# Kernel tuning notes

Measured on AMD Instinct MI355X. Metric: run time of the kernel, lower is better.

The kernel has to match this reference:

```python
import jax, jax.numpy as jnp
import numpy as np

EPS = 1.1920929e-07  # torch.finfo(float32).eps, RMSNorm default eps

def _rms(x, w):
    return x * jax.lax.rsqrt(jnp.mean(x * x, axis=-1, keepdims=True) + EPS) * w

def setup_inputs() -> dict:
    key = jax.random.key(0)
    ks = jax.random.split(key, 8)
    V, E, M, L, B, T = 4096, 1024, 4096, 2, 32, 256
    s = 0.02
    return {
        "tokens": jax.random.randint(ks[0], (B, T), 0, V),
        "targets": jax.random.randint(ks[1], (B, T), 0, V),
        "emb_w": jax.random.normal(ks[2], (V, E), jnp.float32) * s,
        "block_norm_w": jax.random.normal(ks[3], (L, E), jnp.float32) * s,
        "fc1_w": jax.random.normal(ks[4], (L, M, E), jnp.float32) * s,
        "fc1_b": jnp.zeros((L, M), jnp.float32),
        "fc2_w": jax.random.normal(ks[5], (L, E, M), jnp.float32) * s,
        "fc2_b": jnp.zeros((L, E), jnp.float32),
        "norm_w": jax.random.normal(ks[6], (E,), jnp.float32) * s,
        "cur_w": jax.random.normal(ks[7], (E, E), jnp.float32) * s,
        "cur_b": jnp.zeros((E,), jnp.float32),
        "nxt_w": jax.random.normal(jax.random.fold_in(key, 99), (E, E), jnp.float32) * s,
        "nxt_b": jnp.zeros((E,), jnp.float32),
    }

def reference(tokens, targets, emb_w, block_norm_w, fc1_w, fc1_b, fc2_w, fc2_b,
              norm_w, cur_w, cur_b, nxt_w, nxt_b):
    B, T = tokens.shape
    E = emb_w.shape[1]
    L = block_norm_w.shape[0]
    embeds = emb_w[tokens]  # [B,T,E]

    def step(inp, xs):
        tok_emb, tok, tgt = xs  # [B,E], [B], [B]
        inp = tok_emb + inp
        h = inp
        for l in range(L):  # fixed small layer count
            y = jax.nn.silu(_rms(h, block_norm_w[l]) @ fc1_w[l].T + fc1_b[l])
            h = h + y @ fc2_w[l].T + fc2_b[l]
        x = _rms(inp + h, norm_w)
        cur_emb = x @ cur_w.T + cur_b
        nxt_emb = x @ nxt_w.T + nxt_b
        cur_logit = cur_emb @ emb_w.T  # [B,V]
        nxt_logit = nxt_emb @ emb_w.T
        lp_cur = jax.nn.log_softmax(cur_logit, axis=-1)
        lp_nxt = jax.nn.log_softmax(nxt_logit, axis=-1)
        ce_cur = -jnp.mean(jnp.take_along_axis(lp_cur, tok[:, None], axis=1))
        ce_nxt = -jnp.mean(jnp.take_along_axis(lp_nxt, tgt[:, None], axis=1))
        ce = (ce_cur + ce_nxt) / 2
        aux = jnp.mean((cur_emb - inp) ** 2)
        return nxt_emb, (nxt_logit, ce, aux)

    xs = (jnp.swapaxes(embeds, 0, 1), tokens.T, targets.T)
    init = jnp.zeros((B, E), embeds.dtype)
    _, (logits, ces, auxs) = jax.lax.scan(step, init, xs)
    return jnp.swapaxes(logits, 0, 1), jnp.mean(ces), jnp.mean(auxs)
```

## Files before the change

kernel.cpp:

```cpp
#include <hip/hip_runtime.h>
#include <math.h>

#define TT  256
#define BB  32
#define EE  1024
#define MM  4096
#define VV  4096
#define BE  (BB*EE)
#define NROWS (TT*BB)
#define EPSF 1.1920929e-07f

typedef _Float16 h2 __attribute__((ext_vector_type(2)));

__device__ inline float dot2f(h2 a, h2 b, float c) {
#if __has_builtin(__builtin_amdgcn_fdot2)
  return __builtin_amdgcn_fdot2(a, b, c, false);
#else
  return c + (float)a[0] * (float)b[0] + (float)a[1] * (float)b[1];
#endif
}

__device__ inline unsigned ldb_u32(const unsigned* p) {
  return __hip_atomic_load((unsigned*)p, __ATOMIC_RELAXED, __HIP_MEMORY_SCOPE_AGENT);
}
__device__ inline void stb_u32(unsigned* p, unsigned v) {
  __hip_atomic_store(p, v, __ATOMIC_RELAXED, __HIP_MEMORY_SCOPE_AGENT);
}
__device__ inline void stb_f32(float* p, float v) {
  __hip_atomic_store(p, v, __ATOMIC_RELAXED, __HIP_MEMORY_SCOPE_AGENT);
}

__device__ inline void gbar4(unsigned* cnt, int sidx) {
  __syncthreads();
  if (threadIdx.x == 0) {
    unsigned* base = cnt + (size_t)sidx * 17 * 32;
    unsigned* gp = base + (blockIdx.x & 15) * 32;
    unsigned* mp = base + 16 * 32;
    unsigned old = __hip_atomic_fetch_add(gp, 1u, __ATOMIC_RELAXED,
                                          __HIP_MEMORY_SCOPE_AGENT);
    if (old == 15u)
      __hip_atomic_fetch_add(mp, 1u, __ATOMIC_RELAXED, __HIP_MEMORY_SCOPE_AGENT);
    while (__hip_atomic_load(mp, __ATOMIC_RELAXED, __HIP_MEMORY_SCOPE_AGENT) < 16u)
      __builtin_amdgcn_s_sleep(1);
  }
  __syncthreads();
}

template<int NR>
__device__ float fc1like(int tid, int cu,
    const float* __restrict__ src, const float* __restrict__ scl,
    const h2* __restrict__ wl, h2* __restrict__ xs, float* __restrict__ red,
    float* __restrict__ ssrow,
    float* __restrict__ seedDst, const float* __restrict__ seedAdd,
    const float* __restrict__ seedBias) {
  const int b = tid & 31, kq = tid >> 5;
  const int sb = tid >> 4, se = (tid & 15) * 8;
  const int ep0 = (tid & 15) * 4;
  float ssacc = 0.f;
  float acc[NR];
#pragma unroll
  for (int m = 0; m < NR; ++m) acc[m] = 0.f;
  const bool seeder = (seedDst != nullptr) && (cu < 4);

  float4 v0, v1, c0v, c1v;
  auto ldchunk = [&](int c) {
    v0 = *(const float4*)&src[sb * EE + c * 128 + se];
    v1 = *(const float4*)&src[sb * EE + c * 128 + se + 4];
    c0v = *(const float4*)&scl[c * 128 + se];
    c1v = *(const float4*)&scl[c * 128 + se + 4];
  };
  auto flush = [&](int c) {
    h2* dst = xs + (c & 1) * (64 * 33);
    ssacc += v0.x*v0.x + v0.y*v0.y + v0.z*v0.z + v0.w*v0.w
           + v1.x*v1.x + v1.y*v1.y + v1.z*v1.z + v1.w*v1.w;
    h2 p0, p1, p2, p3;
    p0[0]=(_Float16)(v0.x*c0v.x); p0[1]=(_Float16)(v0.y*c0v.y);
    p1[0]=(_Float16)(v0.z*c0v.z); p1[1]=(_Float16)(v0.w*c0v.w);
    p2[0]=(_Float16)(v1.x*c1v.x); p2[1]=(_Float16)(v1.y*c1v.y);
    p3[0]=(_Float16)(v1.z*c1v.z); p3[1]=(_Float16)(v1.w*c1v.w);
    dst[(ep0+0)*33+sb]=p0; dst[(ep0+1)*33+sb]=p1;
    dst[(ep0+2)*33+sb]=p2; dst[(ep0+3)*33+sb]=p3;
    if (seeder && (c >> 1) == cu) {
      int e0 = c * 128 + se;
      float sv[8] = {v0.x,v0.y,v0.z,v0.w,v1.x,v1.y,v1.z,v1.w};
#pragma unroll
      for (int j = 0; j < 8; ++j) {
        float d = sv[j] + seedBias[e0 + j];
        if (seedAdd) d += seedAdd[sb * EE + e0 + j];
        stb_f32(&seedDst[sb * EE + e0 + j], d);
      }
    }
  };
  ldchunk(0); flush(0);
  __syncthreads();
  for (int c = 0; c < 8; ++c) {
    if (c < 7) ldchunk(c + 1);
    const h2* xb = xs + (c & 1) * (64 * 33);
    h2 x0 = xb[(kq*4+0)*33+b], x1 = xb[(kq*4+1)*33+b],
       x2 = xb[(kq*4+2)*33+b], x3 = xb[(kq*4+3)*33+b];
#pragma unroll
    for (int m = 0; m < NR; ++m) {
      const h2* wp = &wl[m * 512 + c * 64 + kq * 4];
      float a = acc[m];
      a = dot2f(x0, wp[0], a); a = dot2f(x1, wp[1], a);
      a = dot2f(x2, wp[2], a); a = dot2f(x3, wp[3], a);
      acc[m] = a;
    }
    if (c < 7) flush(c + 1);
    __syncthreads();
  }
  ssacc += __shfl_xor(ssacc, 8);
  ssacc += __shfl_xor(ssacc, 4);
  ssacc += __shfl_xor(ssacc, 2);
  ssacc += __shfl_xor(ssacc, 1);
  if ((tid & 15) == 0) ssrow[sb] = ssacc;
#pragma unroll
  for (int m = 0; m < NR; ++m) acc[m] += __shfl_xor(acc[m], 32);
  const int wv = tid >> 6, ln = tid & 63;
  if (ln < 32) {
#pragma unroll
    for (int m = 0; m < NR; ++m) red[wv * 544 + ln * 17 + m] = acc[m];
  }
  __syncthreads();
  float z = 0.f;
  if (tid < 32 * NR) {
    const int b2 = (NR == 16) ? (tid >> 4) : (tid >> 2);
    const int m2 = tid & (NR - 1);
#pragma unroll
    for (int w = 0; w < 8; ++w) z += red[w * 544 + b2 * 17 + m2];
  }
  return z;
}

__device__ float fc2like(int tid,
    const unsigned* __restrict__ ysrc,
    const h2* __restrict__ wl, h2* __restrict__ xs, float* __restrict__ red) {
  const int b = tid & 31, kq = tid >> 5;
  const int sb = tid >> 4;
  const int ep0 = (tid & 15) * 4;
  float acc[16];
#pragma unroll
  for (int m = 0; m < 16; ++m) acc[m] = 0.f;
  unsigned q0, q1, q2, q3;
  auto ldchunk = [&](int c) {
    const unsigned* sp = ysrc + (size_t)sb * (MM / 2) + c * 64 + ep0;
    q0 = ldb_u32(sp + 0); q1 = ldb_u32(sp + 1);
    q2 = ldb_u32(sp + 2); q3 = ldb_u32(sp + 3);
  };
  auto flush = [&](int c) {
    h2* dst = xs + (c & 1) * (64 * 33);
    dst[(ep0+0)*33+sb] = __builtin_bit_cast(h2, q0);
    dst[(ep0+1)*33+sb] = __builtin_bit_cast(h2, q1);
    dst[(ep0+2)*33+sb] = __builtin_bit_cast(h2, q2);
    dst[(ep0+3)*33+sb] = __builtin_bit_cast(h2, q3);
  };
  ldchunk(0); flush(0);
  __syncthreads();
  for (int c = 0; c < 8; ++c) {
    if (c < 7) ldchunk(c + 1);
    const h2* xb = xs + (c & 1) * (64 * 33);
    h2 x0 = xb[(kq*4+0)*33+b], x1 = xb[(kq*4+1)*33+b],
       x2 = xb[(kq*4+2)*33+b], x3 = xb[(kq*4+3)*33+b];
#pragma unroll
    for (int m = 0; m < 16; ++m) {
      const h2* wp = &wl[m * 512 + c * 64 + kq * 4];
      float a = acc[m];
      a = dot2f(x0, wp[0], a); a = dot2f(x1, wp[1], a);
      a = dot2f(x2, wp[2], a); a = dot2f(x3, wp[3], a);
      acc[m] = a;
    }
    if (c < 7) flush(c + 1);
    __syncthreads();
  }
#pragma unroll
  for (int m = 0; m < 16; ++m) acc[m] += __shfl_xor(acc[m], 32);
  const int wv = tid >> 6, ln = tid & 63;
  if (ln < 32) {
#pragma unroll
    for (int m = 0; m < 16; ++m) red[wv * 544 + ln * 17 + m] = acc[m];
  }
  __syncthreads();
  const int b2 = tid >> 4, m2 = tid & 15;
  float z = 0.f;
#pragma unroll
  for (int w = 0; w < 8; ++w) z += red[w * 544 + b2 * 17 + m2];
  return z;
}

struct Scan4Params {
  const int* tokens; const float* embw;
  const float* bnw; const float* fc1w; const float* fc1b;
  const float* fc2w; const float* fc2b;
  const float* nw; const float* nxtw; const float* nxtb;
  float* inp_all;
  float* s_all;
  float* hbuf_all;
  float* nxt_all;
  unsigned* yh;
  float* ssS;
  unsigned* cnt;
};

__global__ __launch_bounds__(512, 1) void k_scan4(Scan4Params p) {
  extern __shared__ __align__(16) char smem[];
  h2* w1a = (h2*)smem;
  h2* w1b = (h2*)(smem + 32768);
  h2* w2a = (h2*)(smem + 65536);
  h2* w2b = (h2*)(smem + 98304);
  h2* wn  = (h2*)(smem + 131072);
  h2* xs  = (h2*)(smem + 139264);
  float* red = (float*)(smem + 139264);
  float* ssrow = (float*)(smem + 156672);
  const int tid = threadIdx.x;
  const int cu = blockIdx.x;
  const int cg = cu & 63, ks = cu >> 6;

#pragma unroll 4
  for (int r = 0; r < 16; ++r) {
    float2 f = *(const float2*)&p.fc1w[(size_t)(cu * 16 + r) * EE + tid * 2];
    h2 h; h[0] = (_Float16)f.x; h[1] = (_Float16)f.y;
    w1a[r * 512 + tid] = h;
    float2 g = *(const float2*)&p.fc1w[(size_t)MM * EE +
                                       (size_t)(cu * 16 + r) * EE + tid * 2];
    h2 hb; hb[0] = (_Float16)g.x; hb[1] = (_Float16)g.y;
    w1b[r * 512 + tid] = hb;
    float2 a = *(const float2*)&p.fc2w[(size_t)(cg * 16 + r) * MM +
                                       ks * 1024 + tid * 2];
    h2 ha; ha[0] = (_Float16)a.x; ha[1] = (_Float16)a.y;
    w2a[r * 512 + tid] = ha;
    float2 bb = *(const float2*)&p.fc2w[(size_t)EE * MM +
                                        (size_t)(cg * 16 + r) * MM +
                                        ks * 1024 + tid * 2];
    h2 hc; hc[0] = (_Float16)bb.x; hc[1] = (_Float16)bb.y;
    w2b[r * 512 + tid] = hc;
  }
#pragma unroll
  for (int r = 0; r < 4; ++r) {
    float2 f = *(const float2*)&p.nxtw[(size_t)(cu * 4 + r) * EE + tid * 2];
    h2 h; h[0] = (_Float16)f.x; h[1] = (_Float16)f.y;
    wn[r * 512 + tid] = h;
  }
  __syncthreads();

  int sidx = 0;
  for (int t = 0; t < TT; ++t) {
    const float* inp = p.inp_all + (size_t)t * BE;
    float* hb = p.hbuf_all + (size_t)t * BE;
    float* st = p.s_all + (size_t)t * BE;

    {
      float z = fc1like<16>(tid, cu, inp, p.bnw, w1a, xs, red, ssrow,
                            hb, nullptr, p.fc2b);
      const int b2 = tid >> 4, m2 = tid & 15, gm = cu * 16 + m2;
      float rinv = rsqrtf(ssrow[b2] * (1.f / EE) + EPSF);
      float zz = z * rinv + p.fc1b[gm];
      float yv = zz / (1.f + expf(-zz));
      unsigned bits = (unsigned)__builtin_bit_cast(unsigned short, (_Float16)yv);
      unsigned other = __shfl_xor(bits, 1);
      if ((tid & 1) == 0)
        stb_u32(&p.yh[b2 * (MM / 2) + (gm >> 1)], bits | (other << 16));
    }
    gbar4(p.cnt, sidx++);
    {
      float z = fc2like(tid, p.yh + ks * 512, w2a, xs, red);
      atomicAdd(&hb[(tid >> 4) * EE + cg * 16 + (tid & 15)], z);
    }
    gbar4(p.cnt, sidx++);
    {
      float z = fc1like<16>(tid, cu, hb, p.bnw + EE, w1b, xs, red, ssrow,
                            st, inp, p.fc2b + EE);
      const int b2 = tid >> 4, m2 = tid & 15, gm = cu * 16 + m2;
      float rinv = rsqrtf(ssrow[b2] * (1.f / EE) + EPSF);
      float zz = z * rinv + p.fc1b[MM + gm];
      float yv = zz / (1.f + expf(-zz));
      unsigned bits = (unsigned)__builtin_bit_cast(unsigned short, (_Float16)yv);
      unsigned other = __shfl_xor(bits, 1);
      if ((tid & 1) == 0)
        stb_u32(&p.yh[b2 * (MM / 2) + (gm >> 1)], bits | (other << 16));
    }
    gbar4(p.cnt, sidx++);
    {
      float z = fc2like(tid, p.yh + ks * 512, w2b, xs, red);
      atomicAdd(&st[(tid >> 4) * EE + cg * 16 + (tid & 15)], z);
    }
    gbar4(p.cnt, sidx++);
    {
      float z = fc1like<4>(tid, cu, st, p.nw, wn, xs, red, ssrow,
                           nullptr, nullptr, nullptr);
      if (cu == 0 && tid < 32) p.ssS[t * 32 + tid] = ssrow[tid];
      if (tid < 128) {
        const int b2 = tid >> 2, m2 = tid & 3, gn = cu * 4 + m2;
        float rinv = rsqrtf(ssrow[b2] * (1.f / EE) + EPSF);
        float nv = z * rinv + p.nxtb[gn];
        stb_f32(&p.nxt_all[(size_t)t * BE + b2 * EE + gn], nv);
        if (t + 1 < TT) {
          int tok = p.tokens[b2 * TT + t + 1];
          stb_f32(&p.inp_all[(size_t)(t + 1) * BE + b2 * EE + gn],
                  p.embw[(size_t)tok * EE + gn] + nv);
        }
      }
    }
    gbar4(p.cnt, sidx++);
  }
}


__global__ void k_zero(float* __restrict__ p, int n) {
  int i = blockIdx.x * 256 + threadIdx.x;
  if (i < n) p[i] = 0.f;
}

__global__ void k_init(const int* __restrict__ tokens,
                       const float* __restrict__ embw,
                       float* __restrict__ inp0) {
  int b = blockIdx.x;
  int tok = tokens[b * TT];
  int e = threadIdx.x * 4;
  float4 v = *(const float4*)&embw[(size_t)tok * EE + e];
  *(float4*)&inp0[b * EE + e] = v;
}


__global__ __launch_bounds__(256)
void k_fc1(const float* __restrict__ h, const float* __restrict__ bnw,
           const float* __restrict__ W, const float* __restrict__ bias,
           float* __restrict__ yout, float* __restrict__ initDst,
           const float* __restrict__ initAdd, const float* __restrict__ initBias) {
  __shared__ __align__(16) float Hs[32][68];
  __shared__ __align__(16) float Ws[8][68];
  __shared__ float ssrow[32];
  const int tid = threadIdx.x;
  const int col0 = blockIdx.x * 8;
  const int c = tid & 7;
  const int b = tid >> 3;
  const bool writer = (blockIdx.x == 0);
  float acc = 0.f;
  float ssl[8];
#pragma unroll
  for (int j = 0; j < 8; ++j) ssl[j] = 0.f;
  for (int kc = 0; kc < EE; kc += 64) {
#pragma unroll
    for (int j = 0; j < 8; ++j) {
      int i = tid + j * 256;
      int bb = i >> 6, k = i & 63;
      float v = h[bb * EE + kc + k];
      ssl[j] += v * v;
      Hs[bb][k] = v * bnw[kc + k];
      if (writer) {
        float d = v + initBias[kc + k];
        if (initAdd) d += initAdd[bb * EE + kc + k];
        initDst[bb * EE + kc + k] = d;
      }
    }
#pragma unroll
    for (int j = 0; j < 2; ++j) {
      int i = tid + j * 256;
      int cc = i >> 6, k = i & 63;
      Ws[cc][k] = W[(size_t)(col0 + cc) * EE + kc + k];
    }
    __syncthreads();
#pragma unroll
    for (int k = 0; k < 64; k += 4) {
      float4 w4 = *(const float4*)&Ws[c][k];
      float4 h4 = *(const float4*)&Hs[b][k];
      acc += h4.x * w4.x + h4.y * w4.y + h4.z * w4.z + h4.w * w4.w;
    }
    __syncthreads();
  }
  const int wv = tid >> 6;
#pragma unroll
  for (int j = 0; j < 8; ++j) {
    float v = ssl[j];
#pragma unroll
    for (int off = 32; off > 0; off >>= 1) v += __shfl_xor(v, off);
    if ((tid & 63) == 0) ssrow[wv + 4 * j] = v;
  }
  __syncthreads();
  float rinv = rsqrtf(ssrow[b] * (1.f / EE) + EPSF);
  float z = acc * rinv + bias[col0 + c];
  yout[b * MM + col0 + c] = z / (1.f + expf(-z));
}

__global__ __launch_bounds__(256)
void k_fc2(const float* __restrict__ y, const float* __restrict__ W2,
           float* __restrict__ dest) {
  __shared__ __align__(16) float Ys[32][68];
  __shared__ __align__(16) float Ws[16][68];
  const int tid = threadIdx.x;
  const int cgi = blockIdx.x & 63;
  const int ks = blockIdx.x >> 6;
  const int col0 = cgi * 16;
  const int c = tid & 15;
  const int bq = tid >> 4;
  float acc0 = 0.f, acc1 = 0.f;
  const int kend = ks * 512 + 512;
  for (int kc = ks * 512; kc < kend; kc += 64) {
#pragma unroll
    for (int j = 0; j < 8; ++j) {
      int i = tid + j * 256;
      int bb = i >> 6, k = i & 63;
      Ys[bb][k] = y[bb * MM + kc + k];
    }
#pragma unroll
    for (int j = 0; j < 4; ++j) {
      int i = tid + j * 256;
      int cc = i >> 6, k = i & 63;
      Ws[cc][k] = W2[(size_t)(col0 + cc) * MM + kc + k];
    }
    __syncthreads();
#pragma unroll
    for (int k = 0; k < 64; k += 4) {
      float4 w4 = *(const float4*)&Ws[c][k];
      float4 a4 = *(const float4*)&Ys[bq][k];
      float4 b4 = *(const float4*)&Ys[bq + 16][k];
      acc0 += a4.x * w4.x + a4.y * w4.y + a4.z * w4.z + a4.w * w4.w;
      acc1 += b4.x * w4.x + b4.y * w4.y + b4.z * w4.z + b4.w * w4.w;
    }
    __syncthreads();
  }
  atomicAdd(&dest[bq * EE + col0 + c], acc0);
  atomicAdd(&dest[(bq + 16) * EE + col0 + c], acc1);
}

__global__ __launch_bounds__(256)
void k_nxt(const float* __restrict__ s, const float* __restrict__ nw,
           const float* __restrict__ Wn, const float* __restrict__ nb,
           float* __restrict__ nxt_out, float* __restrict__ ss_out,
           const int* __restrict__ tokens, const float* __restrict__ embw,
           float* __restrict__ inp_next, int tnext) {
  __shared__ __align__(16) float Xs[32][68];
  __shared__ __align__(16) float Ws[8][68];
  __shared__ float ssrow[32];
  const int tid = threadIdx.x;
  const int col0 = blockIdx.x * 8;
  const int c = tid & 7;
  const int b = tid >> 3;
  float acc = 0.f;
  float ssl[8];
#pragma unroll
  for (int j = 0; j < 8; ++j) ssl[j] = 0.f;
  for (int kc = 0; kc < EE; kc += 64) {
#pragma unroll
    for (int j = 0; j < 8; ++j) {
      int i = tid + j * 256;
      int bb = i >> 6, k = i & 63;
      float v = s[bb * EE + kc + k];
      ssl[j] += v * v;
      Xs[bb][k] = v * nw[kc + k];
    }
#pragma unroll
    for (int j = 0; j < 2; ++j) {
      int i = tid + j * 256;
      int cc = i >> 6, k = i & 63;
      Ws[cc][k] = Wn[(size_t)(col0 + cc) * EE + kc + k];
    }
    __syncthreads();
#pragma unroll
    for (int k = 0; k < 64; k += 4) {
      float4 w4 = *(const float4*)&Ws[c][k];
      float4 h4 = *(const float4*)&Xs[b][k];
      acc += h4.x * w4.x + h4.y * w4.y + h4.z * w4.z + h4.w * w4.w;
    }
    __syncthreads();
  }
  const int wv = tid >> 6;
#pragma unroll
  for (int j = 0; j < 8; ++j) {
    float v = ssl[j];
#pragma unroll
    for (int off = 32; off > 0; off >>= 1) v += __shfl_xor(v, off);
    if ((tid & 63) == 0) {
      ssrow[wv + 4 * j] = v;
      if (blockIdx.x == 0) ss_out[wv + 4 * j] = v;
    }
  }
  __syncthreads();
  float rinv = rsqrtf(ssrow[b] * (1.f / EE) + EPSF);
  float nv = acc * rinv + nb[col0 + c];
  nxt_out[b * EE + col0 + c] = nv;
  if (inp_next) {
    int tok = tokens[b * TT + tnext];
    inp_next[b * EE + col0 + c] = embw[(size_t)tok * EE + col0 + c] + nv;
  }
}


__global__ __launch_bounds__(256)
void k_curemb(const float* __restrict__ s_all, const float* __restrict__ ss_s,
              const float* __restrict__ nw, const float* __restrict__ Wc,
              const float* __restrict__ cb, const float* __restrict__ inp_all,
              float* __restrict__ cur_out, float* __restrict__ aux_accum) {
  __shared__ __align__(16) float As[16][68];
  __shared__ __align__(16) float Bs[16][68];
  __shared__ float rr[64];
  __shared__ float wred[4];
  const int tid = threadIdx.x;
  const int rt = blockIdx.x & 127;
  const int ct = blockIdx.x >> 7;
  const int row0 = rt * 64, col0 = ct * 64;
  if (tid < 64) rr[tid] = rsqrtf(ss_s[row0 + tid] * (1.f / EE) + EPSF);
  __syncthreads();
  float acc[4][4];
#pragma unroll
  for (int i = 0; i < 4; ++i)
#pragma unroll
    for (int j = 0; j < 4; ++j) acc[i][j] = 0.f;
  const int tx = tid & 15, ty = tid >> 4;
  for (int kc = 0; kc < EE; kc += 16) {
#pragma unroll
    for (int j = 0; j < 4; ++j) {
      int i = tid + j * 256;
      int k = i & 15, m = i >> 4;
      As[k][m] = s_all[(size_t)(row0 + m) * EE + kc + k] * rr[m] * nw[kc + k];
      Bs[k][m] = Wc[(size_t)(col0 + m) * EE + kc + k];
    }
    __syncthreads();
#pragma unroll
    for (int k = 0; k < 16; ++k) {
      float4 a4 = *(const float4*)&As[k][tx * 4];
      float4 b4 = *(const float4*)&Bs[k][ty * 4];
      acc[0][0] += a4.x*b4.x; acc[0][1] += a4.x*b4.y; acc[0][2] += a4.x*b4.z; acc[0][3] += a4.x*b4.w;
      acc[1][0] += a4.y*b4.x; acc[1][1] += a4.y*b4.y; acc[1][2] += a4.y*b4.z; acc[1][3] += a4.y*b4.w;
      acc[2][0] += a4.z*b4.x; acc[2][1] += a4.z*b4.y; acc[2][2] += a4.z*b4.z; acc[2][3] += a4.z*b4.w;
      acc[3][0] += a4.w*b4.x; acc[3][1] += a4.w*b4.y; acc[3][2] += a4.w*b4.z; acc[3][3] += a4.w*b4.w;
    }
    __syncthreads();
  }
  float auxp = 0.f;
#pragma unroll
  for (int i = 0; i < 4; ++i) {
    int r = row0 + tx * 4 + i;
#pragma unroll
    for (int j = 0; j < 4; ++j) {
      int col = col0 + ty * 4 + j;
      float v = acc[i][j] + cb[col];
      cur_out[(size_t)r * EE + col] = v;
      float d = v - inp_all[(size_t)r * EE + col];
      auxp += d * d;
    }
  }
#pragma unroll
  for (int off = 32; off > 0; off >>= 1) auxp += __shfl_xor(auxp, off);
  if ((tid & 63) == 0) wred[tid >> 6] = auxp;
  __syncthreads();
  if (tid == 0) atomicAdd(aux_accum, wred[0] + wred[1] + wred[2] + wred[3]);
}

__global__ __launch_bounds__(256)
void k_logits(const float* __restrict__ A, const float* __restrict__ embw,
              const int* __restrict__ idxs, float* __restrict__ rowsum,
              float* __restrict__ lidx, float* __restrict__ store) {
  __shared__ __align__(16) float As[16][68];
  __shared__ __align__(16) float Bs[16][68];
  __shared__ float rowpart[64];
  const int tid = threadIdx.x;
  const int rt = blockIdx.x & 127;
  const int ct = blockIdx.x >> 7;
  const int row0 = rt * 64, col0 = ct * 64;
  float acc[4][4];
#pragma unroll
  for (int i = 0; i < 4; ++i)
#pragma unroll
    for (int j = 0; j < 4; ++j) acc[i][j] = 0.f;
  const int tx = tid & 15, ty = tid >> 4;
  for (int kc = 0; kc < EE; kc += 16) {
#pragma unroll
    for (int j = 0; j < 4; ++j) {
      int i = tid + j * 256;
      int k = i & 15, m = i >> 4;
      As[k][m] = A[(size_t)(row0 + m) * EE + kc + k];
      Bs[k][m] = embw[(size_t)(col0 + m) * EE + kc + k];
    }
    __syncthreads();
#pragma unroll
    for (int k = 0; k < 16; ++k) {
      float4 a4 = *(const float4*)&As[k][tx * 4];
      float4 b4 = *(const float4*)&Bs[k][ty * 4];
      acc[0][0] += a4.x*b4.x; acc[0][1] += a4.x*b4.y; acc[0][2] += a4.x*b4.z; acc[0][3] += a4.x*b4.w;
      acc[1][0] += a4.y*b4.x; acc[1][1] += a4.y*b4.y; acc[1][2] += a4.y*b4.z; acc[1][3] += a4.y*b4.w;
      acc[2][0] += a4.z*b4.x; acc[2][1] += a4.z*b4.y; acc[2][2] += a4.z*b4.z; acc[2][3] += a4.z*b4.w;
      acc[3][0] += a4.w*b4.x; acc[3][1] += a4.w*b4.y; acc[3][2] += a4.w*b4.z; acc[3][3] += a4.w*b4.w;
    }
    __syncthreads();
  }
  if (tid < 64) rowpart[tid] = 0.f;
  __syncthreads();
#pragma unroll
  for (int i = 0; i < 4; ++i) {
    int r = row0 + tx * 4 + i;
    int t = r >> 5, bb = r & 31;
    int idx = idxs[bb * TT + t];
    float e0 = expf(acc[i][0]);
    float e1 = expf(acc[i][1]);
    float e2 = expf(acc[i][2]);
    float e3 = expf(acc[i][3]);
    atomicAdd(&rowpart[tx * 4 + i], e0 + e1 + e2 + e3);
    int cbase = col0 + ty * 4;
#pragma unroll
    for (int j = 0; j < 4; ++j)
      if (cbase + j == idx) lidx[r] = acc[i][j];
    if (store) {
      float4 o = make_float4(acc[i][0], acc[i][1], acc[i][2], acc[i][3]);
      *(float4*)(store + ((size_t)bb * TT + t) * VV + cbase) = o;
    }
  }
  __syncthreads();
  if (tid < 64) atomicAdd(&rowsum[row0 + tid], rowpart[tid]);
}

__global__ void k_final(const float* __restrict__ rs_cur,
                        const float* __restrict__ rs_nxt,
                        const float* __restrict__ ltok,
                        const float* __restrict__ ltgt,
                        const float* __restrict__ aux_accum,
                        float* __restrict__ out) {
  float p = 0.f;
  for (int r = threadIdx.x; r < NROWS; r += 256)
    p += (ltok[r] - logf(rs_cur[r])) + (ltgt[r] - logf(rs_nxt[r]));
#pragma unroll
  for (int off = 32; off > 0; off >>= 1) p += __shfl_xor(p, off);
  __shared__ float w[4];
  if ((threadIdx.x & 63) == 0) w[threadIdx.x >> 6] = p;
  __syncthreads();
  if (threadIdx.x == 0) {
    float tot = w[0] + w[1] + w[2] + w[3];
    out[0] = -tot / (2.f * (float)NROWS);
    out[1] = aux_accum[0] * (1.f / ((float)NROWS * EE));
  }
}


extern "C" void kernel_launch(void* const* d_in, const int* in_sizes, int n_in,
                              void* d_out, int out_size, void* d_ws, size_t ws_size,
                              hipStream_t stream) {
  (void)in_sizes; (void)n_in; (void)out_size; (void)ws_size;
  const int*   tokens  = (const int*)d_in[0];
  const int*   targets = (const int*)d_in[1];
  const float* embw    = (const float*)d_in[2];
  const float* bnw     = (const float*)d_in[3];
  const float* fc1w    = (const float*)d_in[4];
  const float* fc1b    = (const float*)d_in[5];
  const float* fc2w    = (const float*)d_in[6];
  const float* fc2b    = (const float*)d_in[7];
  const float* nw      = (const float*)d_in[8];
  const float* curw    = (const float*)d_in[9];
  const float* curb    = (const float*)d_in[10];
  const float* nxtw    = (const float*)d_in[11];
  const float* nxtb    = (const float*)d_in[12];
  float* out = (float*)d_out;

  float* cur_all  = out;
  float* s_all    = out + (size_t)NROWS * EE;
  float* inp_all  = out + 2 * (size_t)NROWS * EE;
  float* hbuf_all = out + 3 * (size_t)NROWS * EE;

  float* ws       = (float*)d_ws;
  float* nxt_all  = ws;
  float* ltok     = ws + 8388608;
  float* ltgt     = ws + 8396800;
  unsigned* yh    = (unsigned*)(ws + 8404992);
  float* rs_cur   = ws + 8470528;
  float* rs_nxt   = ws + 8478720;
  float* auxac    = ws + 8486912;
  unsigned* cnt   = (unsigned*)(ws + 8486944);
  float* ssS      = ws + 9183264;
  float* ybuf     = ws + 9191456;

  const int nzero = (8486944 + 696320) - 8470528;
  k_zero<<<(nzero + 255) / 256, 256, 0, stream>>>(rs_cur, nzero);
  k_init<<<32, 256, 0, stream>>>(tokens, embw, inp_all);

  Scan4Params p;
  p.tokens = tokens; p.embw = embw; p.bnw = bnw;
  p.fc1w = fc1w; p.fc1b = fc1b; p.fc2w = fc2w; p.fc2b = fc2b;
  p.nw = nw; p.nxtw = nxtw; p.nxtb = nxtb;
  p.inp_all = inp_all; p.s_all = s_all; p.hbuf_all = hbuf_all;
  p.nxt_all = nxt_all; p.yh = yh; p.ssS = ssS; p.cnt = cnt;

  const size_t shmem = 156800;
  hipError_t err = hipFuncSetAttribute((const void*)k_scan4,
      hipFuncAttributeMaxDynamicSharedMemorySize, (int)shmem);
  if (err == hipSuccess) {
    void* args[] = { &p };
    err = hipLaunchCooperativeKernel((const void*)k_scan4, dim3(256), dim3(512),
                                     args, shmem, stream);
  }
  if (err != hipSuccess) {
    float* hbuf = hbuf_all;
    for (int t = 0; t < TT; ++t) {
      const float* inp = inp_all + (size_t)t * BE;
      float* s = s_all + (size_t)t * BE;
      k_fc1<<<512, 256, 0, stream>>>(inp, bnw, fc1w, fc1b, ybuf,
                                     hbuf, nullptr, fc2b);
      k_fc2<<<512, 256, 0, stream>>>(ybuf, fc2w, hbuf);
      k_fc1<<<512, 256, 0, stream>>>(hbuf, bnw + EE, fc1w + (size_t)MM * EE,
                                     fc1b + MM, ybuf, s, inp, fc2b + EE);
      k_fc2<<<512, 256, 0, stream>>>(ybuf, fc2w + (size_t)EE * MM, s);
      k_nxt<<<128, 256, 0, stream>>>(s, nw, nxtw, nxtb,
                                     nxt_all + (size_t)t * BE, ssS + t * BB,
                                     tokens, embw,
                                     (t + 1 < TT) ? inp_all + (size_t)(t + 1) * BE : nullptr,
                                     t + 1);
    }
  }

  k_curemb<<<2048, 256, 0, stream>>>(s_all, ssS, nw, curw, curb, inp_all,
                                     cur_all, auxac);
  k_logits<<<8192, 256, 0, stream>>>(cur_all, embw, tokens, rs_cur, ltok, nullptr);
  k_logits<<<8192, 256, 0, stream>>>(nxt_all, embw, targets, rs_nxt, ltgt, out);
  k_final<<<1, 256, 0, stream>>>(rs_cur, rs_nxt, ltok, ltgt, auxac,
                                 out + (size_t)NROWS * VV);
}
```

Measured before the change: 19.41 ms.

## Load GEMV activations directly into registers and fold norm weights into matrices

The fc1/fc2 helpers no longer stage activations through a double-buffered LDS transpose with a barrier per chunk. Each thread now loads all eight chunks of its row slice straight into registers and accumulates there, computing the sum of squares per thread and reducing it through the existing reduction buffer. The RMSNorm scale vectors are folded into the fp16 fc1 and nxt weights once at load time, so the per-step activation scaling is removed. This cuts per-step __syncthreads and LDS traffic but raises register pressure and changes global access to strided per-thread reads.

```diff
diff --git a/kernel.cpp b/kernel.cpp
--- a/kernel.cpp
+++ b/kernel.cpp
@@ -47,79 +47,67 @@
 }
 
 template<int NR>
-__device__ float fc1like(int tid, int cu,
-    const float* __restrict__ src, const float* __restrict__ scl,
-    const h2* __restrict__ wl, h2* __restrict__ xs, float* __restrict__ red,
-    float* __restrict__ ssrow,
+__device__ float fc1reg(int tid, int cu,
+    const float* __restrict__ src, const h2* __restrict__ wl,
+    float* __restrict__ red, float* __restrict__ ssrow,
     float* __restrict__ seedDst, const float* __restrict__ seedAdd,
     const float* __restrict__ seedBias) {
   const int b = tid & 31, kq = tid >> 5;
-  const int sb = tid >> 4, se = (tid & 15) * 8;
-  const int ep0 = (tid & 15) * 4;
-  float ssacc = 0.f;
-  float acc[NR];
-#pragma unroll
-  for (int m = 0; m < NR; ++m) acc[m] = 0.f;
-  const bool seeder = (seedDst != nullptr) && (cu < 4);
-
-  float4 v0, v1, c0v, c1v;
-  auto ldchunk = [&](int c) {
-    v0 = *(const float4*)&src[sb * EE + c * 128 + se];
-    v1 = *(const float4*)&src[sb * EE + c * 128 + se + 4];
-    c0v = *(const float4*)&scl[c * 128 + se];
-    c1v = *(const float4*)&scl[c * 128 + se + 4];
-  };
-  auto flush = [&](int c) {
-    h2* dst = xs + (c & 1) * (64 * 33);
-    ssacc += v0.x*v0.x + v0.y*v0.y + v0.z*v0.z + v0.w*v0.w
-           + v1.x*v1.x + v1.y*v1.y + v1.z*v1.z + v1.w*v1.w;
-    h2 p0, p1, p2, p3;
-    p0[0]=(_Float16)(v0.x*c0v.x); p0[1]=(_Float16)(v0.y*c0v.y);
-    p1[0]=(_Float16)(v0.z*c0v.z); p1[1]=(_Float16)(v0.w*c0v.w);
-    p2[0]=(_Float16)(v1.x*c1v.x); p2[1]=(_Float16)(v1.y*c1v.y);
-    p3[0]=(_Float16)(v1.z*c1v.z); p3[1]=(_Float16)(v1.w*c1v.w);
-    dst[(ep0+0)*33+sb]=p0; dst[(ep0+1)*33+sb]=p1;
-    dst[(ep0+2)*33+sb]=p2; dst[(ep0+3)*33+sb]=p3;
-    if (seeder && (c >> 1) == cu) {
-      int e0 = c * 128 + se;
-      float sv[8] = {v0.x,v0.y,v0.z,v0.w,v1.x,v1.y,v1.z,v1.w};
+  float4 va[8], vb[8];
+#pragma unroll
+  for (int c = 0; c < 8; ++c) {
+    const float* sp = &src[b * EE + c * 128 + kq * 8];
+    va[c] = *(const float4*)sp;
+    vb[c] = *(const float4*)(sp + 4);
+  }
+  float ssp = 0.f;
+  h2 x[8][4];
+#pragma unroll
+  for (int c = 0; c < 8; ++c) {
+    ssp += va[c].x*va[c].x + va[c].y*va[c].y + va[c].z*va[c].z + va[c].w*va[c].w
+         + vb[c].x*vb[c].x + vb[c].y*vb[c].y + vb[c].z*vb[c].z + vb[c].w*vb[c].w;
+    x[c][0][0]=(_Float16)va[c].x; x[c][0][1]=(_Float16)va[c].y;
+    x[c][1][0]=(_Float16)va[c].z; x[c][1][1]=(_Float16)va[c].w;
+    x[c][2][0]=(_Float16)vb[c].x; x[c][2][1]=(_Float16)vb[c].y;
+    x[c][3][0]=(_Float16)vb[c].z; x[c][3][1]=(_Float16)vb[c].w;
+  }
+  if (seedDst && cu < 4) {
+#pragma unroll
+    for (int cc = 0; cc < 2; ++cc) {
+      const int c = cu * 2 + cc;
+      const int e0 = c * 128 + kq * 8;
+      float sv[8] = {va[c].x, va[c].y, va[c].z, va[c].w,
+                     vb[c].x, vb[c].y, vb[c].z, vb[c].w};
 #pragma unroll
       for (int j = 0; j < 8; ++j) {
         float d = sv[j] + seedBias[e0 + j];
-        if (seedAdd) d += seedAdd[sb * EE + e0 + j];
-        stb_f32(&seedDst[sb * EE + e0 + j], d);
+        if (seedAdd) d += seedAdd[b * EE + e0 + j];
+        stb_f32(&seedDst[b * EE + e0 + j], d);
       }
     }
-  };
-  ldchunk(0); flush(0);
-  __syncthreads();
+  }
+  float acc[NR];
+#pragma unroll
+  for (int m = 0; m < NR; ++m) acc[m] = 0.f;
+#pragma unroll
   for (int c = 0; c < 8; ++c) {
-    if (c < 7) ldchunk(c + 1);
-    const h2* xb = xs + (c & 1) * (64 * 33);
-    h2 x0 = xb[(kq*4+0)*33+b], x1 = xb[(kq*4+1)*33+b],
-       x2 = xb[(kq*4+2)*33+b], x3 = xb[(kq*4+3)*33+b];
 #pragma unroll
     for (int m = 0; m < NR; ++m) {
       const h2* wp = &wl[m * 512 + c * 64 + kq * 4];
       float a = acc[m];
-      a = dot2f(x0, wp[0], a); a = dot2f(x1, wp[1], a);
-      a = dot2f(x2, wp[2], a); a = dot2f(x3, wp[3], a);
+      a = dot2f(x[c][0], wp[0], a); a = dot2f(x[c][1], wp[1], a);
+      a = dot2f(x[c][2], wp[2], a); a = dot2f(x[c][3], wp[3], a);
       acc[m] = a;
     }
-    if (c < 7) flush(c + 1);
-    __syncthreads();
-  }
-  ssacc += __shfl_xor(ssacc, 8);
-  ssacc += __shfl_xor(ssacc, 4);
-  ssacc += __shfl_xor(ssacc, 2);
-  ssacc += __shfl_xor(ssacc, 1);
-  if ((tid & 15) == 0) ssrow[sb] = ssacc;
+  }
 #pragma unroll
   for (int m = 0; m < NR; ++m) acc[m] += __shfl_xor(acc[m], 32);
+  ssp += __shfl_xor(ssp, 32);
   const int wv = tid >> 6, ln = tid & 63;
   if (ln < 32) {
 #pragma unroll
     for (int m = 0; m < NR; ++m) red[wv * 544 + ln * 17 + m] = acc[m];
+    red[wv * 544 + ln * 17 + 16] = ssp;
   }
   __syncthreads();
   float z = 0.f;
@@ -129,38 +117,35 @@
 #pragma unroll
     for (int w = 0; w < 8; ++w) z += red[w * 544 + b2 * 17 + m2];
   }
+  if (tid < 32) {
+    float ss = 0.f;
+#pragma unroll
+    for (int w = 0; w < 8; ++w) ss += red[w * 544 + tid * 17 + 16];
+    ssrow[tid] = ss;
+  }
+  __syncthreads();
   return z;
 }
 
-__device__ float fc2like(int tid,
-    const unsigned* __restrict__ ysrc,
-    const h2* __restrict__ wl, h2* __restrict__ xs, float* __restrict__ red) {
+__device__ float fc2reg(int tid, const unsigned* __restrict__ ysrc,
+    const h2* __restrict__ wl, float* __restrict__ red) {
   const int b = tid & 31, kq = tid >> 5;
-  const int sb = tid >> 4;
-  const int ep0 = (tid & 15) * 4;
+  unsigned q[8][4];
+#pragma unroll
+  for (int c = 0; c < 8; ++c) {
+    const unsigned* sp = ysrc + (size_t)b * (MM / 2) + c * 64 + kq * 4;
+    q[c][0] = ldb_u32(sp + 0); q[c][1] = ldb_u32(sp + 1);
+    q[c][2] = ldb_u32(sp + 2); q[c][3] = ldb_u32(sp + 3);
+  }
   float acc[16];
 #pragma unroll
   for (int m = 0; m < 16; ++m) acc[m] = 0.f;
-  unsigned q0, q1, q2, q3;
-  auto ldchunk = [&](int c) {
-    const unsigned* sp = ysrc + (size_t)sb * (MM / 2) + c * 64 + ep0;
-    q0 = ldb_u32(sp + 0); q1 = ldb_u32(sp + 1);
-    q2 = ldb_u32(sp + 2); q3 = ldb_u32(sp + 3);
-  };
-  auto flush = [&](int c) {
-    h2* dst = xs + (c & 1) * (64 * 33);
-    dst[(ep0+0)*33+sb] = __builtin_bit_cast(h2, q0);
-    dst[(ep0+1)*33+sb] = __builtin_bit_cast(h2, q1);
-    dst[(ep0+2)*33+sb] = __builtin_bit_cast(h2, q2);
-    dst[(ep0+3)*33+sb] = __builtin_bit_cast(h2, q3);
-  };
-  ldchunk(0); flush(0);
-  __syncthreads();
+#pragma unroll
   for (int c = 0; c < 8; ++c) {
-    if (c < 7) ldchunk(c + 1);
-    const h2* xb = xs + (c & 1) * (64 * 33);
-    h2 x0 = xb[(kq*4+0)*33+b], x1 = xb[(kq*4+1)*33+b],
-       x2 = xb[(kq*4+2)*33+b], x3 = xb[(kq*4+3)*33+b];
+    h2 x0 = __builtin_bit_cast(h2, q[c][0]);
+    h2 x1 = __builtin_bit_cast(h2, q[c][1]);
+    h2 x2 = __builtin_bit_cast(h2, q[c][2]);
+    h2 x3 = __builtin_bit_cast(h2, q[c][3]);
 #pragma unroll
     for (int m = 0; m < 16; ++m) {
       const h2* wp = &wl[m * 512 + c * 64 + kq * 4];
@@ -169,8 +154,6 @@
       a = dot2f(x2, wp[2], a); a = dot2f(x3, wp[3], a);
       acc[m] = a;
     }
-    if (c < 7) flush(c + 1);
-    __syncthreads();
   }
 #pragma unroll
   for (int m = 0; m < 16; ++m) acc[m] += __shfl_xor(acc[m], 32);
@@ -208,37 +191,41 @@
   h2* w2a = (h2*)(smem + 65536);
   h2* w2b = (h2*)(smem + 98304);
   h2* wn  = (h2*)(smem + 131072);
-  h2* xs  = (h2*)(smem + 139264);
   float* red = (float*)(smem + 139264);
   float* ssrow = (float*)(smem + 156672);
   const int tid = threadIdx.x;
   const int cu = blockIdx.x;
   const int cg = cu & 63, ks = cu >> 6;
 
+  {
+    float2 bn0 = *(const float2*)&p.bnw[tid * 2];
+    float2 bn1 = *(const float2*)&p.bnw[EE + tid * 2];
+    float2 nwv = *(const float2*)&p.nw[tid * 2];
 #pragma unroll 4
-  for (int r = 0; r < 16; ++r) {
-    float2 f = *(const float2*)&p.fc1w[(size_t)(cu * 16 + r) * EE + tid * 2];
-    h2 h; h[0] = (_Float16)f.x; h[1] = (_Float16)f.y;
-    w1a[r * 512 + tid] = h;
-    float2 g = *(const float2*)&p.fc1w[(size_t)MM * EE +
-                                       (size_t)(cu * 16 + r) * EE + tid * 2];
-    h2 hb; hb[0] = (_Float16)g.x; hb[1] = (_Float16)g.y;
-    w1b[r * 512 + tid] = hb;
-    float2 a = *(const float2*)&p.fc2w[(size_t)(cg * 16 + r) * MM +
-                                       ks * 1024 + tid * 2];
-    h2 ha; ha[0] = (_Float16)a.x; ha[1] = (_Float16)a.y;
-    w2a[r * 512 + tid] = ha;
-    float2 bb = *(const float2*)&p.fc2w[(size_t)EE * MM +
-                                        (size_t)(cg * 16 + r) * MM +
-                                        ks * 1024 + tid * 2];
-    h2 hc; hc[0] = (_Float16)bb.x; hc[1] = (_Float16)bb.y;
-    w2b[r * 512 + tid] = hc;
-  }
-#pragma unroll
-  for (int r = 0; r < 4; ++r) {
-    float2 f = *(const float2*)&p.nxtw[(size_t)(cu * 4 + r) * EE + tid * 2];
-    h2 h; h[0] = (_Float16)f.x; h[1] = (_Float16)f.y;
-    wn[r * 512 + tid] = h;
+    for (int r = 0; r < 16; ++r) {
+      float2 f = *(const float2*)&p.fc1w[(size_t)(cu * 16 + r) * EE + tid * 2];
+      h2 h; h[0] = (_Float16)(f.x * bn0.x); h[1] = (_Float16)(f.y * bn0.y);
+      w1a[r * 512 + tid] = h;
+      float2 g = *(const float2*)&p.fc1w[(size_t)MM * EE +
+                                         (size_t)(cu * 16 + r) * EE + tid * 2];
+      h2 hb; hb[0] = (_Float16)(g.x * bn1.x); hb[1] = (_Float16)(g.y * bn1.y);
+      w1b[r * 512 + tid] = hb;
+      float2 a = *(const float2*)&p.fc2w[(size_t)(cg * 16 + r) * MM +
+                                         ks * 1024 + tid * 2];
+      h2 ha; ha[0] = (_Float16)a.x; ha[1] = (_Float16)a.y;
+      w2a[r * 512 + tid] = ha;
+      float2 bb = *(const float2*)&p.fc2w[(size_t)EE * MM +
+                                          (size_t)(cg * 16 + r) * MM +
+                                          ks * 1024 + tid * 2];
+      h2 hc; hc[0] = (_Float16)bb.x; hc[1] = (_Float16)bb.y;
+      w2b[r * 512 + tid] = hc;
+    }
+#pragma unroll
+    for (int r = 0; r < 4; ++r) {
+      float2 f = *(const float2*)&p.nxtw[(size_t)(cu * 4 + r) * EE + tid * 2];
+      h2 h; h[0] = (_Float16)(f.x * nwv.x); h[1] = (_Float16)(f.y * nwv.y);
+      wn[r * 512 + tid] = h;
+    }
   }
   __syncthreads();
 
@@ -249,8 +236,7 @@
     float* st = p.s_all + (size_t)t * BE;
 
     {
-      float z = fc1like<16>(tid, cu, inp, p.bnw, w1a, xs, red, ssrow,
-                            hb, nullptr, p.fc2b);
+      float z = fc1reg<16>(tid, cu, inp, w1a, red, ssrow, hb, nullptr, p.fc2b);
       const int b2 = tid >> 4, m2 = tid & 15, gm = cu * 16 + m2;
       float rinv = rsqrtf(ssrow[b2] * (1.f / EE) + EPSF);
       float zz = z * rinv + p.fc1b[gm];
@@ -262,13 +248,12 @@
     }
     gbar4(p.cnt, sidx++);
     {
-      float z = fc2like(tid, p.yh + ks * 512, w2a, xs, red);
+      float z = fc2reg(tid, p.yh + ks * 512, w2a, red);
       atomicAdd(&hb[(tid >> 4) * EE + cg * 16 + (tid & 15)], z);
     }
     gbar4(p.cnt, sidx++);
     {
-      float z = fc1like<16>(tid, cu, hb, p.bnw + EE, w1b, xs, red, ssrow,
-                            st, inp, p.fc2b + EE);
+      float z = fc1reg<16>(tid, cu, hb, w1b, red, ssrow, st, inp, p.fc2b + EE);
       const int b2 = tid >> 4, m2 = tid & 15, gm = cu * 16 + m2;
       float rinv = rsqrtf(ssrow[b2] * (1.f / EE) + EPSF);
       float zz = z * rinv + p.fc1b[MM + gm];
@@ -280,13 +265,13 @@
     }
     gbar4(p.cnt, sidx++);
     {
-      float z = fc2like(tid, p.yh + ks * 512, w2b, xs, red);
+      float z = fc2reg(tid, p.yh + ks * 512, w2b, red);
       atomicAdd(&st[(tid >> 4) * EE + cg * 16 + (tid & 15)], z);
     }
     gbar4(p.cnt, sidx++);
     {
-      float z = fc1like<4>(tid, cu, st, p.nw, wn, xs, red, ssrow,
-                           nullptr, nullptr, nullptr);
+      float z = fc1reg<4>(tid, cu, st, wn, red, ssrow,
+                          nullptr, nullptr, nullptr);
       if (cu == 0 && tid < 32) p.ssS[t * 32 + tid] = ssrow[tid];
       if (tid < 128) {
         const int b2 = tid >> 2, m2 = tid & 3, gn = cu * 4 + m2;
```

Measured after the change: 27.78 ms. 1.43x slower.

## Use fp16 dot2 GEMMs for cur-emb and logits, spread seed stores across CUs

Applied to the files above, without the earlier changes.

The cur_emb and logits tiled GEMMs now convert their fp32 inputs to packed fp16 pairs in shared memory and accumulate with the fdot2 instruction. This halves shared-memory traffic and instruction count per MAC. Separately, the seeding writes in fc1like are spread across many CUs and threads (4 floats each) instead of being concentrated in the first 4 CUs, which balances the serial tail in the persistent kernel. Risks include reduced precision in the logits and log-softmax path from fp16 rounding of the inputs.

```diff
diff --git a/kernel.cpp b/kernel.cpp
--- a/kernel.cpp
+++ b/kernel.cpp
@@ -60,7 +60,9 @@
   float acc[NR];
 #pragma unroll
   for (int m = 0; m < NR; ++m) acc[m] = 0.f;
-  const bool seeder = (seedDst != nullptr) && (cu < 4);
+  const int seedChunk = cu >> 5;
+  const int seedOff = (cu & 1) * 4;
+  const bool seeder = (seedDst != nullptr) && ((tid & 15) == ((cu & 31) >> 1));
 
   float4 v0, v1, c0v, c1v;
   auto ldchunk = [&](int c) {
@@ -80,15 +82,25 @@
     p3[0]=(_Float16)(v1.z*c1v.z); p3[1]=(_Float16)(v1.w*c1v.w);
     dst[(ep0+0)*33+sb]=p0; dst[(ep0+1)*33+sb]=p1;
     dst[(ep0+2)*33+sb]=p2; dst[(ep0+3)*33+sb]=p3;
-    if (seeder && (c >> 1) == cu) {
-      int e0 = c * 128 + se;
-      float sv[8] = {v0.x,v0.y,v0.z,v0.w,v1.x,v1.y,v1.z,v1.w};
-#pragma unroll
-      for (int j = 0; j < 8; ++j) {
-        float d = sv[j] + seedBias[e0 + j];
-        if (seedAdd) d += seedAdd[sb * EE + e0 + j];
-        stb_f32(&seedDst[sb * EE + e0 + j], d);
+    if (seeder && c == seedChunk) {
+      const int e0 = c * 128 + se + seedOff;
+      float a0, a1, a2, a3;
+      if (seedOff == 0) { a0 = v0.x; a1 = v0.y; a2 = v0.z; a3 = v0.w; }
+      else              { a0 = v1.x; a1 = v1.y; a2 = v1.z; a3 = v1.w; }
+      float d0 = a0 + seedBias[e0 + 0];
+      float d1 = a1 + seedBias[e0 + 1];
+      float d2 = a2 + seedBias[e0 + 2];
+      float d3 = a3 + seedBias[e0 + 3];
+      if (seedAdd) {
+        d0 += seedAdd[sb * EE + e0 + 0];
+        d1 += seedAdd[sb * EE + e0 + 1];
+        d2 += seedAdd[sb * EE + e0 + 2];
+        d3 += seedAdd[sb * EE + e0 + 3];
       }
+      stb_f32(&seedDst[sb * EE + e0 + 0], d0);
+      stb_f32(&seedDst[sb * EE + e0 + 1], d1);
+      stb_f32(&seedDst[sb * EE + e0 + 2], d2);
+      stb_f32(&seedDst[sb * EE + e0 + 3], d3);
     }
   };
   ldchunk(0); flush(0);
@@ -490,8 +502,8 @@
               const float* __restrict__ nw, const float* __restrict__ Wc,
               const float* __restrict__ cb, const float* __restrict__ inp_all,
               float* __restrict__ cur_out, float* __restrict__ aux_accum) {
-  __shared__ __align__(16) float As[16][68];
-  __shared__ __align__(16) float Bs[16][68];
+  __shared__ __align__(16) h2 Ah[8 * 68];
+  __shared__ __align__(16) h2 Bh[8 * 68];
   __shared__ float rr[64];
   __shared__ float wred[4];
   const int tid = threadIdx.x;
@@ -508,21 +520,33 @@
   const int tx = tid & 15, ty = tid >> 4;
   for (int kc = 0; kc < EE; kc += 16) {
 #pragma unroll
-    for (int j = 0; j < 4; ++j) {
-      int i = tid + j * 256;
-      int k = i & 15, m = i >> 4;
-      As[k][m] = s_all[(size_t)(row0 + m) * EE + kc + k] * rr[m] * nw[kc + k];
-      Bs[k][m] = Wc[(size_t)(col0 + m) * EE + kc + k];
-    }
-    __syncthreads();
-#pragma unroll
-    for (int k = 0; k < 16; ++k) {
-      float4 a4 = *(const float4*)&As[k][tx * 4];
-      float4 b4 = *(const float4*)&Bs[k][ty * 4];
-      acc[0][0] += a4.x*b4.x; acc[0][1] += a4.x*b4.y; acc[0][2] += a4.x*b4.z; acc[0][3] += a4.x*b4.w;
-      acc[1][0] += a4.y*b4.x; acc[1][1] += a4.y*b4.y; acc[1][2] += a4.y*b4.z; acc[1][3] += a4.y*b4.w;
-      acc[2][0] += a4.z*b4.x; acc[2][1] += a4.z*b4.y; acc[2][2] += a4.z*b4.z; acc[2][3] += a4.z*b4.w;
-      acc[3][0] += a4.w*b4.x; acc[3][1] += a4.w*b4.y; acc[3][2] += a4.w*b4.z; acc[3][3] += a4.w*b4.w;
+    for (int j = 0; j < 2; ++j) {
+      int idx = tid + j * 256;
+      int kp = idx & 7, m = idx >> 3;
+      float2 f = *(const float2*)&s_all[(size_t)(row0 + m) * EE + kc + 2 * kp];
+      float2 n2 = *(const float2*)&nw[kc + 2 * kp];
+      float r = rr[m];
+      h2 hv; hv[0] = (_Float16)(f.x * r * n2.x); hv[1] = (_Float16)(f.y * r * n2.y);
+      Ah[kp * 68 + m] = hv;
+      float2 w2 = *(const float2*)&Wc[(size_t)(col0 + m) * EE + kc + 2 * kp];
+      h2 hw; hw[0] = (_Float16)w2.x; hw[1] = (_Float16)w2.y;
+      Bh[kp * 68 + m] = hw;
+    }
+    __syncthreads();
+#pragma unroll
+    for (int kp = 0; kp < 8; ++kp) {
+      h2 a0 = Ah[kp*68 + tx*4 + 0], a1 = Ah[kp*68 + tx*4 + 1];
+      h2 a2 = Ah[kp*68 + tx*4 + 2], a3 = Ah[kp*68 + tx*4 + 3];
+      h2 b0 = Bh[kp*68 + ty*4 + 0], b1 = Bh[kp*68 + ty*4 + 1];
+      h2 b2 = Bh[kp*68 + ty*4 + 2], b3 = Bh[kp*68 + ty*4 + 3];
+      acc[0][0]=dot2f(a0,b0,acc[0][0]); acc[0][1]=dot2f(a0,b1,acc[0][1]);
+      acc[0][2]=dot2f(a0,b2,acc[0][2]); acc[0][3]=dot2f(a0,b3,acc[0][3]);
+      acc[1][0]=dot2f(a1,b0,acc[1][0]); acc[1][1]=dot2f(a1,b1,acc[1][1]);
+      acc[1][2]=dot2f(a1,b2,acc[1][2]); acc[1][3]=dot2f(a1,b3,acc[1][3]);
+      acc[2][0]=dot2f(a2,b0,acc[2][0]); acc[2][1]=dot2f(a2,b1,acc[2][1]);
+      acc[2][2]=dot2f(a2,b2,acc[2][2]); acc[2][3]=dot2f(a2,b3,acc[2][3]);
+      acc[3][0]=dot2f(a3,b0,acc[3][0]); acc[3][1]=dot2f(a3,b1,acc[3][1]);
+      acc[3][2]=dot2f(a3,b2,acc[3][2]); acc[3][3]=dot2f(a3,b3,acc[3][3]);
     }
     __syncthreads();
   }
@@ -550,8 +574,8 @@
 void k_logits(const float* __restrict__ A, const float* __restrict__ embw,
               const int* __restrict__ idxs, float* __restrict__ rowsum,
               float* __restrict__ lidx, float* __restrict__ store) {
-  __shared__ __align__(16) float As[16][68];
-  __shared__ __align__(16) float Bs[16][68];
+  __shared__ __align__(16) h2 Ah[8 * 68];
+  __shared__ __align__(16) h2 Bh[8 * 68];
   __shared__ float rowpart[64];
   const int tid = threadIdx.x;
   const int rt = blockIdx.x & 127;
@@ -565,21 +589,31 @@
   const int tx = tid & 15, ty = tid >> 4;
   for (int kc = 0; kc < EE; kc += 16) {
 #pragma unroll
-    for (int j = 0; j < 4; ++j) {
-      int i = tid + j * 256;
-      int k = i & 15, m = i >> 4;
-      As[k][m] = A[(size_t)(row0 + m) * EE + kc + k];
-      Bs[k][m] = embw[(size_t)(col0 + m) * EE + kc + k];
-    }
-    __syncthreads();
-#pragma unroll
-    for (int k = 0; k < 16; ++k) {
-      float4 a4 = *(const float4*)&As[k][tx * 4];
-      float4 b4 = *(const float4*)&Bs[k][ty * 4];
-      acc[0][0] += a4.x*b4.x; acc[0][1] += a4.x*b4.y; acc[0][2] += a4.x*b4.z; acc[0][3] += a4.x*b4.w;
-      acc[1][0] += a4.y*b4.x; acc[1][1] += a4.y*b4.y; acc[1][2] += a4.y*b4.z; acc[1][3] += a4.y*b4.w;
-      acc[2][0] += a4.z*b4.x; acc[2][1] += a4.z*b4.y; acc[2][2] += a4.z*b4.z; acc[2][3] += a4.z*b4.w;
-      acc[3][0] += a4.w*b4.x; acc[3][1] += a4.w*b4.y; acc[3][2] += a4.w*b4.z; acc[3][3] += a4.w*b4.w;
+    for (int j = 0; j < 2; ++j) {
+      int idx = tid + j * 256;
+      int kp = idx & 7, m = idx >> 3;
+      float2 f = *(const float2*)&A[(size_t)(row0 + m) * EE + kc + 2 * kp];
+      h2 hv; hv[0] = (_Float16)f.x; hv[1] = (_Float16)f.y;
+      Ah[kp * 68 + m] = hv;
+      float2 w2 = *(const float2*)&embw[(size_t)(col0 + m) * EE + kc + 2 * kp];
+      h2 hw; hw[0] = (_Float16)w2.x; hw[1] = (_Float16)w2.y;
+      Bh[kp * 68 + m] = hw;
+    }
+    __syncthreads();
+#pragma unroll
+    for (int kp = 0; kp < 8; ++kp) {
+      h2 a0 = Ah[kp*68 + tx*4 + 0], a1 = Ah[kp*68 + tx*4 + 1];
+      h2 a2 = Ah[kp*68 + tx*4 + 2], a3 = Ah[kp*68 + tx*4 + 3];
+      h2 b0 = Bh[kp*68 + ty*4 + 0], b1 = Bh[kp*68 + ty*4 + 1];
+      h2 b2 = Bh[kp*68 + ty*4 + 2], b3 = Bh[kp*68 + ty*4 + 3];
+      acc[0][0]=dot2f(a0,b0,acc[0][0]); acc[0][1]=dot2f(a0,b1,acc[0][1]);
+      acc[0][2]=dot2f(a0,b2,acc[0][2]); acc[0][3]=dot2f(a0,b3,acc[0][3]);
+      acc[1][0]=dot2f(a1,b0,acc[1][0]); acc[1][1]=dot2f(a1,b1,acc[1][1]);
+      acc[1][2]=dot2f(a1,b2,acc[1][2]); acc[1][3]=dot2f(a1,b3,acc[1][3]);
+      acc[2][0]=dot2f(a2,b0,acc[2][0]); acc[2][1]=dot2f(a2,b1,acc[2][1]);
+      acc[2][2]=dot2f(a2,b2,acc[2][2]); acc[2][3]=dot2f(a2,b3,acc[2][3]);
+      acc[3][0]=dot2f(a3,b0,acc[3][0]); acc[3][1]=dot2f(a3,b1,acc[3][1]);
+      acc[3][2]=dot2f(a3,b2,acc[3][2]); acc[3][3]=dot2f(a3,b3,acc[3][3]);
     }
     __syncthreads();
   }
```

New measurement: 17.34 ms (median of 2 runs). -10.7%, faster.
